# Performance work log

Measured on AMD Instinct MI355X. Metric: run time of the kernel, lower is better.

Reference implementation:

```python
import jax, jax.numpy as jnp
import numpy as np

U = I = 100000  # user/item vocab (set equal; __init__ swaps them anyway)
P = 50          # position_len
D = 64          # hidden_units_u == hidden_units_i
B = 8192        # batch
H = 50          # history length


def _attn(data, key, W, b):
    # data: [B,D], key: [B,H,D]; Linear(2D,1) -> Tanh -> Softmax over H
    attn_in = jnp.concatenate([jnp.broadcast_to(data[:, None, :], key.shape), key], axis=-1)  # [B,H,2D]
    w = jax.nn.softmax(jnp.tanh(attn_in @ W + b), axis=1)  # [B,H,1]
    return jnp.sum(w * key, axis=1)  # [B,D]


def setup_inputs() -> dict:
    key = jax.random.key(0)
    ks = jax.random.split(key, 24)
    emb = lambda i, shape: jax.random.normal(ks[i], shape, jnp.float32) * 0.05
    uni = lambda i, shape: jax.random.uniform(ks[i], shape, jnp.float32, -1.0, 1.0)
    ri = lambda i, shape, hi: jax.random.randint(ks[i], shape, 0, hi, jnp.int32)
    return {
        "user1": ri(0, (B,), U), "item1": ri(1, (B,), I),
        "user2": ri(2, (B,), U), "item2": ri(3, (B,), I),
        "u_his": ri(4, (B, H), I), "u_pos": ri(5, (B, H), P), "u_his_mask": ri(6, (B, H), 2),
        "i_his": ri(7, (B, H), U), "i_pos": ri(8, (B, H), P), "i_his_mask": ri(9, (B, H), 2),
        "user1_emb": emb(10, (U, D)), "item1_emb": emb(11, (I, D)),
        "user1_bias": uni(12, (U,)), "item1_bias": uni(13, (I,)),
        "u_pos_emb": emb(14, (P, D)),
        "user2_emb": emb(15, (U, D)), "item2_emb": emb(16, (I, D)),
        "user2_bias": uni(17, (U,)), "item2_bias": uni(18, (I,)),
        "i_pos_emb": emb(19, (P, D)),
        "attn_u_W": emb(20, (2 * D, 1)), "attn_u_b": emb(21, (1,)),
        "attn_i_W": emb(22, (2 * D, 1)), "attn_i_b": emb(23, (1,)),
    }


def _forward(user1_emb, item1_emb, user1_bias, item1_bias, u_pos_emb,
             user2_emb, item2_emb, user2_bias, item2_bias, i_pos_emb,
             attn_u_W, attn_u_b, attn_i_W, attn_i_b,
             user1, item1, user2, item2,
             u_his, u_pos, u_his_mask, i_his, i_pos, i_his_mask):
    sg = jax.lax.stop_gradient
    mu = (u_his_mask != 0).astype(jnp.float32)[..., None]  # [B,H,1]
    mi = (i_his_mask != 0).astype(jnp.float32)[..., None]

    # branch 1 (shared-sign s, detached r)
    u1s = user1_emb[user1]; i1s = item1_emb[item1]
    u1s_b = user1_bias[user1]; i1s_b = item1_bias[item1]
    u1r = sg(user2_emb[user1]); i1r = sg(item2_emb[item1])
    u1r_b = sg(user2_bias[user1]); i1r_b = sg(item2_bias[item1])
    u_hiss = item1_emb[u_his] * mu            # [B,H,D], masked-zero
    i_hisr = sg(user2_emb[i_his]) * mi
    u_poss = u_pos_emb[u_pos] * mu
    i_posr = sg(i_pos_emb[i_pos]) * mi
    u_ds = _attn(i1s, u_hiss + u_poss, attn_u_W, attn_u_b)
    i_dr = _attn(u1r, i_hisr + i_posr, attn_i_W, attn_i_b)
    logits_us = u1s_b + i1s_b + jnp.sum((u_ds + i1s) * u1s, axis=1)
    logits_ir = u1r_b + i1r_b + jnp.sum((i_dr + i1r) * u1r, axis=1)

    # branch 2 (roles swapped)
    u2s = user2_emb[user2]; i2s = item2_emb[item2]
    u2s_b = user2_bias[user2]; i2s_b = item2_bias[item2]
    u2r = sg(user1_emb[user2]); i2r = sg(item1_emb[item2])
    u2r_b = sg(user1_bias[user2]); i2r_b = sg(item1_bias[item2])
    u_hisr = sg(item1_emb[u_his]) * mu
    i_hiss = user2_emb[i_his] * mi
    u_posr = sg(u_pos_emb[u_pos]) * mu
    i_poss = i_pos_emb[i_pos] * mi
    u_dr = _attn(i1r, u_hisr + u_posr, attn_u_W, attn_u_b)
    i_ds = _attn(u1s, i_hiss + i_poss, attn_i_W, attn_i_b)
    logits_ur = u2r_b + i2r_b + jnp.sum((u_dr + i2r) * u2r, axis=1)
    logits_is = u2s_b + i2s_b + jnp.sum((i_ds + i2s) * u2s, axis=1)

    loss_reg1 = jnp.sum(u1s ** 2) + jnp.sum(i1s ** 2) + jnp.sum(u_hiss ** 2)
    loss_reg2 = jnp.sum(u2s ** 2) + jnp.sum(i2s ** 2) + jnp.sum(i_hiss ** 2)
    return (logits_us, logits_ir, logits_ur, logits_is, loss_reg1, loss_reg2)


def reference(user1, item1, user2, item2, u_his, u_pos, u_his_mask, i_his, i_pos, i_his_mask,
              user1_emb, item1_emb, user1_bias, item1_bias, u_pos_emb,
              user2_emb, item2_emb, user2_bias, item2_bias, i_pos_emb,
              attn_u_W, attn_u_b, attn_i_W, attn_i_b):
    return _forward(user1_emb, item1_emb, user1_bias, item1_bias, u_pos_emb,
                    user2_emb, item2_emb, user2_bias, item2_bias, i_pos_emb,
                    attn_u_W, attn_u_b, attn_i_W, attn_i_b,
                    user1, item1, user2, item2,
                    u_his, u_pos, u_his_mask, i_his, i_pos, i_his_mask)
```

## Files before the change

### kernel.cpp

```cpp
#include <hip/hip_runtime.h>

#define NB 8192
#define NH 50
#define ND 64

__device__ __forceinline__ float wsum(float v) {
#pragma unroll
    for (int o = 32; o > 0; o >>= 1) v += __shfl_xor(v, o, 64);
    return v;
}

__device__ __forceinline__ float tanh_fast(float x) {
    const float e = __expf(2.0f * x);
    return (e - 1.0f) * __builtin_amdgcn_rcpf(e + 1.0f);
}

__global__ __launch_bounds__(256, 8) void fwd_kernel(
    const int* __restrict__ user1, const int* __restrict__ item1,
    const int* __restrict__ user2, const int* __restrict__ item2,
    const int* __restrict__ u_his, const int* __restrict__ u_pos, const int* __restrict__ u_mask,
    const int* __restrict__ i_his, const int* __restrict__ i_pos, const int* __restrict__ i_mask,
    const float* __restrict__ user1_emb, const float* __restrict__ item1_emb,
    const float* __restrict__ user1_bias, const float* __restrict__ item1_bias,
    const float* __restrict__ u_pos_emb,
    const float* __restrict__ user2_emb, const float* __restrict__ item2_emb,
    const float* __restrict__ user2_bias, const float* __restrict__ item2_bias,
    const float* __restrict__ i_pos_emb,
    const float* __restrict__ attn_u_W, const float* __restrict__ attn_u_b,
    const float* __restrict__ attn_i_W, const float* __restrict__ attn_i_b,
    float* __restrict__ out, float* __restrict__ ws)
{
    const int wave = threadIdx.x >> 6;
    const int d = threadIdx.x & 63;
    const int b = __builtin_amdgcn_readfirstlane(blockIdx.x * 2 + (wave >> 1));
    const bool iw = (wave & 1);

    const int iu1 = user1[b], ii1 = item1[b], iu2 = user2[b], ii2 = item2[b];

    const int*   his  = iw ? i_his  : u_his;
    const int*   posa = iw ? i_pos  : u_pos;
    const int*   msk  = iw ? i_mask : u_mask;
    const float* ktab = iw ? user2_emb : item1_emb;
    const float* ptab = iw ? i_pos_emb : u_pos_emb;
    const float* W    = iw ? attn_i_W  : attn_u_W;
    const float  bb   = iw ? attn_i_b[0] : attn_u_b[0];

    const float* qa_tab = iw ? user2_emb : item1_emb;
    const float* qb_tab = iw ? user1_emb : item2_emb;
    const int    qidx   = iw ? iu1 : ii1;
    const float qa = qa_tab[(size_t)qidx * ND + d];
    const float qb = qb_tab[(size_t)qidx * ND + d];
    const float Wq = W[d], Wk = W[ND + d];
    const float cq_a = wsum(qa * Wq) + bb;
    const float cq_b = wsum(qb * Wq) + bb;

    int hidx = 0, hpos = 0;
    bool act = false;
    if (d < NH) {
        hidx = his[b * NH + d];
        hpos = posa[b * NH + d];
        act  = (msk[b * NH + d] != 0);
    }
    const unsigned long long bal = __ballot(act);
    const int nact = __builtin_amdgcn_readfirstlane(__popcll(bal));
    const int below = __builtin_amdgcn_mbcnt_hi(
        (unsigned)(bal >> 32), __builtin_amdgcn_mbcnt_lo((unsigned)bal, 0));
    const int tgt = (act ? below : 63) << 2;
    const int idx_c = __builtin_amdgcn_ds_permute(tgt, hidx);
    const int pos_c = __builtin_amdgcn_ds_permute(tgt, hpos);

    float o_a = 0.0f, o_b = 0.0f, den_a = 0.0f, den_b = 0.0f, reg = 0.0f;
#pragma unroll 4
    for (int h = 0; h < nact; ++h) {
        const int ih = __builtin_amdgcn_readlane(idx_c, h);
        const int ip = __builtin_amdgcn_readlane(pos_c, h);
        const float kv = ktab[(size_t)ih * ND + d];
        const float pv = ptab[(size_t)ip * ND + d];
        const float k = kv + pv;
        reg += kv * kv;
        const float s = wsum(k * Wk);
        const float ea = __expf(tanh_fast(cq_a + s));
        const float eb = __expf(tanh_fast(cq_b + s));
        o_a += ea * k;  den_a += ea;
        o_b += eb * k;  den_b += eb;
    }
    den_a += (float)(NH - nact) * __expf(tanh_fast(cq_a));
    den_b += (float)(NH - nact) * __expf(tanh_fast(cq_b));
    o_a *= __builtin_amdgcn_rcpf(den_a);
    o_b *= __builtin_amdgcn_rcpf(den_b);

    const float pa = iw ? item2_emb[(size_t)ii1 * ND + d] : user1_emb[(size_t)iu1 * ND + d];
    const float add_a = iw ? pa : qa;
    const float mul_a = iw ? qa : pa;
    const float add_b = (iw ? item2_emb : item1_emb)[(size_t)ii2 * ND + d];
    const float mul_b = (iw ? user2_emb : user1_emb)[(size_t)iu2 * ND + d];

    const float l_a = wsum((o_a + add_a) * mul_a);
    const float l_b = wsum((o_b + add_b) * mul_b);
    const float rv = iw ? (mul_b * mul_b + add_b * add_b) : (mul_a * mul_a + qa * qa);
    const float r = wsum(rv + reg);

    const float* ub = iw ? user2_bias : user1_bias;
    const float* ib = iw ? item2_bias : item1_bias;
    if (d == 0) {
        out[(iw ? NB : 0) + b]          = ub[iu1] + ib[ii1] + l_a;
        out[(iw ? 3 * NB : 2 * NB) + b] = ub[iu2] + ib[ii2] + l_b;
        ws[(iw ? NB : 0) + b] = r;
    }
}

__global__ void reduce_kernel(const float* __restrict__ ws, float* __restrict__ out) {
    float a = 0.0f, c = 0.0f;
    for (int i = threadIdx.x; i < NB; i += 256) {
        a += ws[i];
        c += ws[NB + i];
    }
    a = wsum(a);
    c = wsum(c);
    __shared__ float sa[4], sc[4];
    const int w = threadIdx.x >> 6, d = threadIdx.x & 63;
    if (d == 0) { sa[w] = a; sc[w] = c; }
    __syncthreads();
    if (threadIdx.x == 0) {
        out[4 * NB]     = sa[0] + sa[1] + sa[2] + sa[3];
        out[4 * NB + 1] = sc[0] + sc[1] + sc[2] + sc[3];
    }
}

extern "C" void kernel_launch(void* const* d_in, const int* in_sizes, int n_in,
                              void* d_out, int out_size, void* d_ws, size_t ws_size,
                              hipStream_t stream) {
    const int* user1 = (const int*)d_in[0];
    const int* item1 = (const int*)d_in[1];
    const int* user2 = (const int*)d_in[2];
    const int* item2 = (const int*)d_in[3];
    const int* u_his = (const int*)d_in[4];
    const int* u_pos = (const int*)d_in[5];
    const int* u_msk = (const int*)d_in[6];
    const int* i_his = (const int*)d_in[7];
    const int* i_pos = (const int*)d_in[8];
    const int* i_msk = (const int*)d_in[9];
    const float* user1_emb  = (const float*)d_in[10];
    const float* item1_emb  = (const float*)d_in[11];
    const float* user1_bias = (const float*)d_in[12];
    const float* item1_bias = (const float*)d_in[13];
    const float* u_pos_emb  = (const float*)d_in[14];
    const float* user2_emb  = (const float*)d_in[15];
    const float* item2_emb  = (const float*)d_in[16];
    const float* user2_bias = (const float*)d_in[17];
    const float* item2_bias = (const float*)d_in[18];
    const float* i_pos_emb  = (const float*)d_in[19];
    const float* attn_u_W = (const float*)d_in[20];
    const float* attn_u_b = (const float*)d_in[21];
    const float* attn_i_W = (const float*)d_in[22];
    const float* attn_i_b = (const float*)d_in[23];
    float* out = (float*)d_out;
    float* ws  = (float*)d_ws;

    fwd_kernel<<<NB / 2, 256, 0, stream>>>(
        user1, item1, user2, item2,
        u_his, u_pos, u_msk, i_his, i_pos, i_msk,
        user1_emb, item1_emb, user1_bias, item1_bias, u_pos_emb,
        user2_emb, item2_emb, user2_bias, item2_bias, i_pos_emb,
        attn_u_W, attn_u_b, attn_i_W, attn_i_b,
        out, ws);
    reduce_kernel<<<1, 256, 0, stream>>>(ws, out);
}
```

Measured before the change: 219.2 us.

## Precompute key-weight dot products per table row and hoist softmax out of loop

```diff
diff --git a/kernel.cpp b/kernel.cpp
--- a/kernel.cpp
+++ b/kernel.cpp
@@ -15,7 +15,146 @@
     return (e - 1.0f) * __builtin_amdgcn_rcpf(e + 1.0f);
 }
 
+__global__ __launch_bounds__(256, 8) void kw_kernel(
+    const float* __restrict__ t0, const float* __restrict__ t1,
+    const float* __restrict__ t2, const float* __restrict__ t3,
+    const float* __restrict__ w0, const float* __restrict__ w1,
+    const float* __restrict__ w2, const float* __restrict__ w3,
+    float* __restrict__ o0, float* __restrict__ o1,
+    float* __restrict__ o2, float* __restrict__ o3,
+    int r0, int r1, int r2, int r3,
+    int b1, int b2, int b3)
+{
+    const int blk = blockIdx.x;
+    const float* tab; const float* W; float* o; int rows, base;
+    if (blk < b1)      { tab = t0; W = w0; o = o0; rows = r0; base = blk; }
+    else if (blk < b2) { tab = t1; W = w1; o = o1; rows = r1; base = blk - b1; }
+    else if (blk < b3) { tab = t2; W = w2; o = o2; rows = r2; base = blk - b2; }
+    else               { tab = t3; W = w3; o = o3; rows = r3; base = blk - b3; }
+    const int lane = threadIdx.x & 63;
+    const int wv = threadIdx.x >> 6;
+    const int sub = lane >> 4, j = lane & 15;
+    const int row = base * 16 + wv * 4 + sub;
+    const int rowc = min(row, rows - 1);
+    const float4 v = *(const float4*)(tab + (size_t)rowc * ND + j * 4);
+    const float4 w = *(const float4*)(W + j * 4);
+    float p = v.x * w.x + v.y * w.y + v.z * w.z + v.w * w.w;
+    p += __shfl_xor(p, 1, 64);
+    p += __shfl_xor(p, 2, 64);
+    p += __shfl_xor(p, 4, 64);
+    p += __shfl_xor(p, 8, 64);
+    if (j == 0 && row < rows) o[row] = p;
+}
+
 __global__ __launch_bounds__(256, 8) void fwd_kernel(
+    const int* __restrict__ user1, const int* __restrict__ item1,
+    const int* __restrict__ user2, const int* __restrict__ item2,
+    const int* __restrict__ u_his, const int* __restrict__ u_pos, const int* __restrict__ u_mask,
+    const int* __restrict__ i_his, const int* __restrict__ i_pos, const int* __restrict__ i_mask,
+    const float* __restrict__ user1_emb, const float* __restrict__ item1_emb,
+    const float* __restrict__ user1_bias, const float* __restrict__ item1_bias,
+    const float* __restrict__ u_pos_emb,
+    const float* __restrict__ user2_emb, const float* __restrict__ item2_emb,
+    const float* __restrict__ user2_bias, const float* __restrict__ item2_bias,
+    const float* __restrict__ i_pos_emb,
+    const float* __restrict__ attn_u_W, const float* __restrict__ attn_u_b,
+    const float* __restrict__ attn_i_W, const float* __restrict__ attn_i_b,
+    const float* __restrict__ KWu, const float* __restrict__ KWi,
+    const float* __restrict__ PWu, const float* __restrict__ PWi,
+    float* __restrict__ out, float* __restrict__ ws)
+{
+    const int wave = threadIdx.x >> 6;
+    const int d = threadIdx.x & 63;
+    const int b = __builtin_amdgcn_readfirstlane(blockIdx.x * 2 + (wave >> 1));
+    const bool iw = (wave & 1);
+
+    const int iu1 = user1[b], ii1 = item1[b], iu2 = user2[b], ii2 = item2[b];
+
+    const int*   his  = iw ? i_his  : u_his;
+    const int*   posa = iw ? i_pos  : u_pos;
+    const int*   msk  = iw ? i_mask : u_mask;
+    const float* ktab = iw ? user2_emb : item1_emb;
+    const float* ptab = iw ? i_pos_emb : u_pos_emb;
+    const float* W    = iw ? attn_i_W  : attn_u_W;
+    const float  bb   = iw ? attn_i_b[0] : attn_u_b[0];
+    const float* KW   = iw ? KWi : KWu;
+    const float* PW   = iw ? PWi : PWu;
+
+    const float* qa_tab = iw ? user2_emb : item1_emb;
+    const float* qb_tab = iw ? user1_emb : item2_emb;
+    const int    qidx   = iw ? iu1 : ii1;
+    const float qa = qa_tab[(size_t)qidx * ND + d];
+    const float qb = qb_tab[(size_t)qidx * ND + d];
+    const float Wq = W[d];
+    const float cq_a = wsum(qa * Wq) + bb;
+    const float cq_b = wsum(qb * Wq) + bb;
+    const float e0_a = __expf(tanh_fast(cq_a));
+    const float e0_b = __expf(tanh_fast(cq_b));
+
+    int hidx = 0, hpos = 0;
+    bool act = false;
+    if (d < NH) {
+        hidx = his[b * NH + d];
+        hpos = posa[b * NH + d];
+        act  = (msk[b * NH + d] != 0);
+    }
+    const float s = KW[hidx] + PW[hpos];
+    float e_a = 0.0f, e_b = 0.0f;
+    if (d < NH) {
+        e_a = act ? __expf(tanh_fast(cq_a + s)) : e0_a;
+        e_b = act ? __expf(tanh_fast(cq_b + s)) : e0_b;
+    }
+    const float den_a = wsum(e_a);
+    const float den_b = wsum(e_b);
+
+    const unsigned long long bal = __ballot(act);
+    const int nact = __builtin_amdgcn_readfirstlane(__popcll(bal));
+    const int below = __builtin_amdgcn_mbcnt_hi(
+        (unsigned)(bal >> 32), __builtin_amdgcn_mbcnt_lo((unsigned)bal, 0));
+    const int tgt = (act ? below : 63) << 2;
+    const int idx_c = __builtin_amdgcn_ds_permute(tgt, hidx);
+    const int pos_c = __builtin_amdgcn_ds_permute(tgt, hpos);
+    const int ea_c  = __builtin_amdgcn_ds_permute(tgt, __float_as_int(e_a));
+    const int eb_c  = __builtin_amdgcn_ds_permute(tgt, __float_as_int(e_b));
+
+    float o_a = 0.0f, o_b = 0.0f, reg = 0.0f;
+#pragma unroll 4
+    for (int h = 0; h < nact; ++h) {
+        const int ih = __builtin_amdgcn_readlane(idx_c, h);
+        const int ip = __builtin_amdgcn_readlane(pos_c, h);
+        const float ea = __int_as_float(__builtin_amdgcn_readlane(ea_c, h));
+        const float eb = __int_as_float(__builtin_amdgcn_readlane(eb_c, h));
+        const float kv = ktab[(size_t)ih * ND + d];
+        const float pv = ptab[ip * ND + d];
+        const float k = kv + pv;
+        o_a += ea * k;
+        o_b += eb * k;
+        reg += kv * kv;
+    }
+    o_a *= __builtin_amdgcn_rcpf(den_a);
+    o_b *= __builtin_amdgcn_rcpf(den_b);
+
+    const float pa = iw ? item2_emb[(size_t)ii1 * ND + d] : user1_emb[(size_t)iu1 * ND + d];
+    const float add_a = iw ? pa : qa;
+    const float mul_a = iw ? qa : pa;
+    const float add_b = (iw ? item2_emb : item1_emb)[(size_t)ii2 * ND + d];
+    const float mul_b = (iw ? user2_emb : user1_emb)[(size_t)iu2 * ND + d];
+
+    const float l_a = wsum((o_a + add_a) * mul_a);
+    const float l_b = wsum((o_b + add_b) * mul_b);
+    const float rv = iw ? (mul_b * mul_b + add_b * add_b) : (mul_a * mul_a + qa * qa);
+    const float r = wsum(rv + reg);
+
+    const float* ub = iw ? user2_bias : user1_bias;
+    const float* ib = iw ? item2_bias : item1_bias;
+    if (d == 0) {
+        out[(iw ? NB : 0) + b]          = ub[iu1] + ib[ii1] + l_a;
+        out[(iw ? 3 * NB : 2 * NB) + b] = ub[iu2] + ib[ii2] + l_b;
+        ws[(iw ? NB : 0) + b] = r;
+    }
+}
+
+__global__ __launch_bounds__(256, 8) void fwd_fallback(
     const int* __restrict__ user1, const int* __restrict__ item1,
     const int* __restrict__ user2, const int* __restrict__ item2,
     const int* __restrict__ u_his, const int* __restrict__ u_pos, const int* __restrict__ u_mask,
@@ -36,7 +175,6 @@
     const bool iw = (wave & 1);
 
     const int iu1 = user1[b], ii1 = item1[b], iu2 = user2[b], ii2 = item2[b];
-
     const int*   his  = iw ? i_his  : u_his;
     const int*   posa = iw ? i_pos  : u_pos;
     const int*   msk  = iw ? i_mask : u_mask;
@@ -44,7 +182,6 @@
     const float* ptab = iw ? i_pos_emb : u_pos_emb;
     const float* W    = iw ? attn_i_W  : attn_u_W;
     const float  bb   = iw ? attn_i_b[0] : attn_u_b[0];
-
     const float* qa_tab = iw ? user2_emb : item1_emb;
     const float* qb_tab = iw ? user1_emb : item2_emb;
     const int    qidx   = iw ? iu1 : ii1;
@@ -94,12 +231,10 @@
     const float mul_a = iw ? qa : pa;
     const float add_b = (iw ? item2_emb : item1_emb)[(size_t)ii2 * ND + d];
     const float mul_b = (iw ? user2_emb : user1_emb)[(size_t)iu2 * ND + d];
-
     const float l_a = wsum((o_a + add_a) * mul_a);
     const float l_b = wsum((o_b + add_b) * mul_b);
     const float rv = iw ? (mul_b * mul_b + add_b * add_b) : (mul_a * mul_a + qa * qa);
     const float r = wsum(rv + reg);
-
     const float* ub = iw ? user2_bias : user1_bias;
     const float* ib = iw ? item2_bias : item1_bias;
     if (d == 0) {
@@ -157,12 +292,44 @@
     float* out = (float*)d_out;
     float* ws  = (float*)d_ws;
 
-    fwd_kernel<<<NB / 2, 256, 0, stream>>>(
-        user1, item1, user2, item2,
-        u_his, u_pos, u_msk, i_his, i_pos, i_msk,
-        user1_emb, item1_emb, user1_bias, item1_bias, u_pos_emb,
-        user2_emb, item2_emb, user2_bias, item2_bias, i_pos_emb,
-        attn_u_W, attn_u_b, attn_i_W, attn_i_b,
-        out, ws);
+    const int I_rows = in_sizes[11] / ND;
+    const int U_rows = in_sizes[15] / ND;
+    const int P_rows = in_sizes[14] / ND;
+
+    float* KWu = ws + 2 * NB;
+    float* KWi = KWu + I_rows;
+    float* PWu = KWi + U_rows;
+    float* PWi = PWu + 64;
+    const size_t need = (size_t)(2 * NB + I_rows + U_rows + 128) * sizeof(float);
+
+    if (ws_size >= need) {
+        const int nb0 = (I_rows + 15) / 16;
+        const int nb1 = (U_rows + 15) / 16;
+        const int nb2 = (P_rows + 15) / 16;
+        const int b1 = nb0, b2 = nb0 + nb1, b3 = nb0 + nb1 + nb2;
+        const int total = b3 + nb2;
+        kw_kernel<<<total, 256, 0, stream>>>(
+            item1_emb, user2_emb, u_pos_emb, i_pos_emb,
+            attn_u_W + ND, attn_i_W + ND, attn_u_W + ND, attn_i_W + ND,
+            KWu, KWi, PWu, PWi,
+            I_rows, U_rows, P_rows, P_rows,
+            b1, b2, b3);
+        fwd_kernel<<<NB / 2, 256, 0, stream>>>(
+            user1, item1, user2, item2,
+            u_his, u_pos, u_msk, i_his, i_pos, i_msk,
+            user1_emb, item1_emb, user1_bias, item1_bias, u_pos_emb,
+            user2_emb, item2_emb, user2_bias, item2_bias, i_pos_emb,
+            attn_u_W, attn_u_b, attn_i_W, attn_i_b,
+            KWu, KWi, PWu, PWi,
+            out, ws);
+    } else {
+        fwd_fallback<<<NB / 2, 256, 0, stream>>>(
+            user1, item1, user2, item2,
+            u_his, u_pos, u_msk, i_his, i_pos, i_msk,
+            user1_emb, item1_emb, user1_bias, item1_bias, u_pos_emb,
+            user2_emb, item2_emb, user2_bias, item2_bias, i_pos_emb,
+            attn_u_W, attn_u_b, attn_i_W, attn_i_b,
+            out, ws);
+    }
     reduce_kernel<<<1, 256, 0, stream>>>(ws, out);
 }
```

After: 207.8 us. -5.2%, faster.

## Process four history rows per wave with float4 loads and parallel reduction

Applied to the files above, without the earlier changes.

```diff
diff --git a/kernel.cpp b/kernel.cpp
--- a/kernel.cpp
+++ b/kernel.cpp
@@ -10,12 +10,24 @@
     return v;
 }
 
+__device__ __forceinline__ float gsum16(float v) {
+    v += __shfl_xor(v, 1, 64);
+    v += __shfl_xor(v, 2, 64);
+    v += __shfl_xor(v, 4, 64);
+    v += __shfl_xor(v, 8, 64);
+    return v;
+}
+
 __device__ __forceinline__ float tanh_fast(float x) {
     const float e = __expf(2.0f * x);
     return (e - 1.0f) * __builtin_amdgcn_rcpf(e + 1.0f);
 }
 
-__global__ __launch_bounds__(256, 8) void fwd_kernel(
+__device__ __forceinline__ float dot4(const float4 a, const float4 b) {
+    return a.x * b.x + a.y * b.y + a.z * b.z + a.w * b.w;
+}
+
+__global__ __launch_bounds__(256, 4) void fwd_kernel(
     const int* __restrict__ user1, const int* __restrict__ item1,
     const int* __restrict__ user2, const int* __restrict__ item2,
     const int* __restrict__ u_his, const int* __restrict__ u_pos, const int* __restrict__ u_mask,
@@ -34,6 +46,13 @@
     const int d = threadIdx.x & 63;
     const int b = __builtin_amdgcn_readfirstlane(blockIdx.x * 2 + (wave >> 1));
     const bool iw = (wave & 1);
+    const int sub = d >> 4;
+    const int col = (d & 15) * 4;
+
+    if (blockIdx.x == 0 && threadIdx.x == 0) {
+        out[4 * NB] = 0.0f;
+        out[4 * NB + 1] = 0.0f;
+    }
 
     const int iu1 = user1[b], ii1 = item1[b], iu2 = user2[b], ii2 = item2[b];
 
@@ -45,15 +64,6 @@
     const float* W    = iw ? attn_i_W  : attn_u_W;
     const float  bb   = iw ? attn_i_b[0] : attn_u_b[0];
 
-    const float* qa_tab = iw ? user2_emb : item1_emb;
-    const float* qb_tab = iw ? user1_emb : item2_emb;
-    const int    qidx   = iw ? iu1 : ii1;
-    const float qa = qa_tab[(size_t)qidx * ND + d];
-    const float qb = qb_tab[(size_t)qidx * ND + d];
-    const float Wq = W[d], Wk = W[ND + d];
-    const float cq_a = wsum(qa * Wq) + bb;
-    const float cq_b = wsum(qb * Wq) + bb;
-
     int hidx = 0, hpos = 0;
     bool act = false;
     if (d < NH) {
@@ -61,6 +71,24 @@
         hpos = posa[b * NH + d];
         act  = (msk[b * NH + d] != 0);
     }
+
+    const float* qa_tab = iw ? user2_emb : item1_emb;
+    const float* qb_tab = iw ? user1_emb : item2_emb;
+    const int    qidx   = iw ? iu1 : ii1;
+    const float4 qa4 = *(const float4*)(qa_tab + (size_t)qidx * ND + col);
+    const float4 qb4 = *(const float4*)(qb_tab + (size_t)qidx * ND + col);
+    const float4 pa4 = *(const float4*)((iw ? item2_emb : user1_emb) +
+                                        (size_t)(iw ? ii1 : iu1) * ND + col);
+    const float4 ab4 = *(const float4*)((iw ? item2_emb : item1_emb) + (size_t)ii2 * ND + col);
+    const float4 mb4 = *(const float4*)((iw ? user2_emb : user1_emb) + (size_t)iu2 * ND + col);
+    const float4 Wq4 = *(const float4*)(W + col);
+    const float4 Wk4 = *(const float4*)(W + ND + col);
+
+    const float cq_a = wsum(dot4(qa4, Wq4)) * 0.25f + bb;
+    const float cq_b = wsum(dot4(qb4, Wq4)) * 0.25f + bb;
+    const float e0_a = __expf(tanh_fast(cq_a));
+    const float e0_b = __expf(tanh_fast(cq_b));
+
     const unsigned long long bal = __ballot(act);
     const int nact = __builtin_amdgcn_readfirstlane(__popcll(bal));
     const int below = __builtin_amdgcn_mbcnt_hi(
@@ -69,36 +97,44 @@
     const int idx_c = __builtin_amdgcn_ds_permute(tgt, hidx);
     const int pos_c = __builtin_amdgcn_ds_permute(tgt, hpos);
 
-    float o_a = 0.0f, o_b = 0.0f, den_a = 0.0f, den_b = 0.0f, reg = 0.0f;
+    float4 oa = make_float4(0.f, 0.f, 0.f, 0.f);
+    float4 ob = make_float4(0.f, 0.f, 0.f, 0.f);
+    float den_a_acc = 0.0f, den_b_acc = 0.0f, reg = 0.0f;
 #pragma unroll 4
-    for (int h = 0; h < nact; ++h) {
-        const int ih = __builtin_amdgcn_readlane(idx_c, h);
-        const int ip = __builtin_amdgcn_readlane(pos_c, h);
-        const float kv = ktab[(size_t)ih * ND + d];
-        const float pv = ptab[(size_t)ip * ND + d];
-        const float k = kv + pv;
-        reg += kv * kv;
-        const float s = wsum(k * Wk);
-        const float ea = __expf(tanh_fast(cq_a + s));
-        const float eb = __expf(tanh_fast(cq_b + s));
-        o_a += ea * k;  den_a += ea;
-        o_b += eb * k;  den_b += eb;
-    }
-    den_a += (float)(NH - nact) * __expf(tanh_fast(cq_a));
-    den_b += (float)(NH - nact) * __expf(tanh_fast(cq_b));
-    o_a *= __builtin_amdgcn_rcpf(den_a);
-    o_b *= __builtin_amdgcn_rcpf(den_b);
-
-    const float pa = iw ? item2_emb[(size_t)ii1 * ND + d] : user1_emb[(size_t)iu1 * ND + d];
-    const float add_a = iw ? pa : qa;
-    const float mul_a = iw ? qa : pa;
-    const float add_b = (iw ? item2_emb : item1_emb)[(size_t)ii2 * ND + d];
-    const float mul_b = (iw ? user2_emb : user1_emb)[(size_t)iu2 * ND + d];
-
-    const float l_a = wsum((o_a + add_a) * mul_a);
-    const float l_b = wsum((o_b + add_b) * mul_b);
-    const float rv = iw ? (mul_b * mul_b + add_b * add_b) : (mul_a * mul_a + qa * qa);
-    const float r = wsum(rv + reg);
+    for (int base = 0; base < nact; base += 4) {
+        const int sid = base + sub;
+        const bool v = sid < nact;
+        const int off = (v ? sid : 0) << 2;
+        const int ih = __builtin_amdgcn_ds_bpermute(off, idx_c);
+        const int ip = __builtin_amdgcn_ds_bpermute(off, pos_c);
+        const float4 kv = *(const float4*)(ktab + (size_t)ih * ND + col);
+        const float4 pv = *(const float4*)(ptab + ip * ND + col);
+        float4 k;
+        k.x = kv.x + pv.x; k.y = kv.y + pv.y; k.z = kv.z + pv.z; k.w = kv.w + pv.w;
+        const float s = gsum16(dot4(k, Wk4));
+        float ea = __expf(tanh_fast(cq_a + s));
+        float eb = __expf(tanh_fast(cq_b + s));
+        ea = v ? ea : 0.0f;
+        eb = v ? eb : 0.0f;
+        oa.x += ea * k.x; oa.y += ea * k.y; oa.z += ea * k.z; oa.w += ea * k.w;
+        ob.x += eb * k.x; ob.y += eb * k.y; ob.z += eb * k.z; ob.w += eb * k.w;
+        den_a_acc += ea;
+        den_b_acc += eb;
+        reg += v ? dot4(kv, kv) : 0.0f;
+    }
+
+    const float den_a = wsum(den_a_acc) * 0.0625f + (float)(NH - nact) * e0_a;
+    const float den_b = wsum(den_b_acc) * 0.0625f + (float)(NH - nact) * e0_b;
+
+    const float rd_a = __builtin_amdgcn_rcpf(den_a);
+    const float rd_b = __builtin_amdgcn_rcpf(den_b);
+    const float4 aa4 = iw ? pa4 : qa4;
+    const float4 ma4 = iw ? qa4 : pa4;
+    const float l_a = wsum(dot4(oa, ma4) * rd_a + 0.25f * dot4(aa4, ma4));
+    const float l_b = wsum(dot4(ob, mb4) * rd_b + 0.25f * dot4(ab4, mb4));
+    const float rv = iw ? (dot4(mb4, mb4) + dot4(ab4, ab4))
+                        : (dot4(ma4, ma4) + dot4(qa4, qa4));
+    const float r = wsum(reg + 0.25f * rv);
 
     const float* ub = iw ? user2_bias : user1_bias;
     const float* ib = iw ? item2_bias : item1_bias;
@@ -109,22 +145,18 @@
     }
 }
 
-__global__ void reduce_kernel(const float* __restrict__ ws, float* __restrict__ out) {
-    float a = 0.0f, c = 0.0f;
-    for (int i = threadIdx.x; i < NB; i += 256) {
-        a += ws[i];
-        c += ws[NB + i];
-    }
-    a = wsum(a);
-    c = wsum(c);
+__global__ __launch_bounds__(256, 8) void reduce2_kernel(
+    const float* __restrict__ ws, float* __restrict__ out)
+{
+    const int i = blockIdx.x * 256 + threadIdx.x;
+    const float a = wsum(ws[i]);
+    const float c = wsum(ws[NB + i]);
     __shared__ float sa[4], sc[4];
     const int w = threadIdx.x >> 6, d = threadIdx.x & 63;
     if (d == 0) { sa[w] = a; sc[w] = c; }
     __syncthreads();
-    if (threadIdx.x == 0) {
-        out[4 * NB]     = sa[0] + sa[1] + sa[2] + sa[3];
-        out[4 * NB + 1] = sc[0] + sc[1] + sc[2] + sc[3];
-    }
+    if (threadIdx.x == 0)  atomicAdd(&out[4 * NB],     sa[0] + sa[1] + sa[2] + sa[3]);
+    if (threadIdx.x == 64) atomicAdd(&out[4 * NB + 1], sc[0] + sc[1] + sc[2] + sc[3]);
 }
 
 extern "C" void kernel_launch(void* const* d_in, const int* in_sizes, int n_in,
@@ -164,5 +196,5 @@
         user2_emb, item2_emb, user2_bias, item2_bias, i_pos_emb,
         attn_u_W, attn_u_b, attn_i_W, attn_i_b,
         out, ws);
-    reduce_kernel<<<1, 256, 0, stream>>>(ws, out);
-}
+    reduce2_kernel<<<32, 256, 0, stream>>>(ws, out);
+}
```

Result: faster. 185.7 us (-15.3%).
